# Performance work log

Hardware: AMD Instinct MI355X
Metric: run time of the kernel (lower is better)

## Reference

```python
import jax, jax.numpy as jnp
import numpy as np
from jax import lax

OC = 128      # out_channels
KS = 7        # kernel_size
STRIDE = 2
IMG = 224     # image_size
NS = 7        # num_scales
PAD = KS // 2 # 3
MAXS = 2      # max_scale
EPS = 1e-5
OUT = IMG // STRIDE  # 112
B = 32
DN = ('NCHW', 'OIHW', 'NCHW')


def _windows():
    # Mirrors the torch __init__ window construction (float32 linspace like torch).
    scales = np.linspace(2.0, 1.0, NS, dtype=np.float32)
    borders = np.linspace(0, IMG // 2, NS + 1).astype(np.int64)
    iw = np.empty((NS, 4, 4), dtype=np.int64)
    for s in range(NS):
        a, b = borders[s], borders[s + 1]
        c, d = IMG - b, IMG - a
        iw[s] = np.array([[a, a, b, c], [b, a, d, b], [c, b, d, d], [a, c, c, d]])
    ow = iw // STRIDE  # output windows
    iwp = iw + PAD * MAXS
    iwp = np.stack([(iwp[s].astype(np.float32) / scales[s]).astype(np.int64) for s in range(NS)])
    iwp[:, :, :2] -= PAD
    iwp[:, :, 2:] += PAD
    return iwp, ow

IWP, OW = _windows()


def _bn(x, g, b):
    # BatchNorm2d in training mode: biased batch stats over (N, H, W)
    m = jnp.mean(x, axis=(0, 2, 3), keepdims=True)
    v = jnp.var(x, axis=(0, 2, 3), keepdims=True)
    return g[None, :, None, None] * (x - m) * lax.rsqrt(v + EPS) + b[None, :, None, None]


def _forward(inp, conv_w, gamma1, beta1, conv2_w, gamma2, beta2):
    n = inp.shape[0]
    x = jnp.pad(inp, ((0, 0), (0, 0), (PAD, PAD), (PAD, PAD)))  # ConstantPad2d(3, 0)
    out = jnp.zeros((n, OC, OUT, OUT), inp.dtype)
    for s in range(NS):
        for w in range(4):
            ti, li, bi, ri = (int(v) for v in IWP[s, w])
            crop = x[:, :, ti:bi, li:ri]
            # torch interpolate(bilinear, antialias) to the crop's own size is the identity,
            # since input_window_sizes == (bi-ti, ri-li) exactly.
            f = lax.conv_general_dilated(crop, conv_w, (STRIDE, STRIDE), 'VALID',
                                         dimension_numbers=DN)
            to, lo, bo, ro = (int(v) for v in OW[s, w])
            oh, owid = bo - to, ro - lo
            fh, fw = f.shape[2], f.shape[3]
            # torch 'nearest' (size-based): src = floor(i * in / out)
            ih = (np.arange(oh) * fh) // oh
            iwd = (np.arange(owid) * fw) // owid
            up = f[:, :, ih][:, :, :, iwd]
            out = out.at[:, :, to:bo, lo:ro].set(up)
    h = jax.nn.relu(_bn(out, gamma1, beta1))
    # MaxPool2d(kernel=3, stride=2, padding=1) -> pads with -inf
    h = lax.reduce_window(h, jnp.asarray(-jnp.inf, h.dtype), lax.max,
                          (1, 1, 3, 3), (1, 1, 2, 2),
                          ((0, 0), (0, 0), (1, 1), (1, 1)))
    h = lax.conv_general_dilated(h, conv2_w, (1, 1), ((1, 1), (1, 1)),
                                 dimension_numbers=DN)
    return jax.nn.relu(_bn(h, gamma2, beta2))


def setup_inputs() -> dict:
    key = jax.random.key(0)
    k0, k1, k2 = jax.random.split(key, 3)
    inp = jax.random.normal(k0, (B, 3, IMG, IMG), jnp.float32)
    conv_w = jax.random.normal(k1, (OC, 3, KS, KS), jnp.float32) * 0.05
    conv2_w = jax.random.normal(k2, (OC, OC, 3, 3), jnp.float32) * 0.03
    return {
        'inp': inp,
        'conv_w': conv_w,
        'gamma1': jnp.ones((OC,), jnp.float32),
        'beta1': jnp.zeros((OC,), jnp.float32),
        'conv2_w': conv2_w,
        'gamma2': jnp.ones((OC,), jnp.float32),
        'beta2': jnp.zeros((OC,), jnp.float32),
    }


def reference(inp, conv_w, gamma1, beta1, conv2_w, gamma2, beta2):
    return _forward(inp, conv_w, gamma1, beta1, conv2_w, gamma2, beta2)
```

## Files before the change

kernel.cpp:

```cpp
#include <hip/hip_runtime.h>
#include <hip/hip_bf16.h>
#include <cstdint>

#define IMGSZ 224
#define OUTSZ 112
#define POOLSZ 56
#define OCN 128
#define BN_ 32
#define PIX1 (OUTSZ*OUTSZ)
#define PIX2 (POOLSZ*POOLSZ)
#define HP 58
#define HSTRIDE (HP*HP*OCN)
#define PW 240
#define PH 233
#define PPL (PH*PW)
#define K1C 192

typedef float f32x4 __attribute__((ext_vector_type(4)));
typedef short bf16x8 __attribute__((ext_vector_type(8)));
struct alignas(4) u4a { unsigned x, y, z, w; };

__device__ inline short f2bf(float v) {
    __hip_bfloat16 h = __float2bfloat16(v);
    return *(short*)&h;
}
__device__ inline unsigned pack2bf(float a, float b) {
    return (unsigned short)f2bf(a) | ((unsigned)(unsigned short)f2bf(b) << 16);
}
__device__ inline float bf2f(short s) {
    return __uint_as_float(((unsigned)(unsigned short)s) << 16);
}
__device__ inline bf16x8 ldb8(const short* p) {
    u4a t = *(const u4a*)p;
    union { u4a u; bf16x8 v; } c; c.u = t; return c.v;
}
__device__ inline void gload16(const short* g, short* l) {
    __builtin_amdgcn_global_load_lds((const __attribute__((address_space(1))) void*)g,
                                     (__attribute__((address_space(3))) void*)l, 16, 0, 0);
}

template<int CTRL>
__device__ inline float dppf(float v) {
    return __int_as_float(__builtin_amdgcn_update_dpp(0, __float_as_int(v), CTRL, 0xF, 0xF, true));
}
__device__ inline float rowsum16(float v) {
    v += dppf<0xB1>(v);
    v += dppf<0x4E>(v);
    v += dppf<0x141>(v);
    v += dppf<0x140>(v);
    return v;
}

__global__ __launch_bounds__(256) void k_setup(const float* __restrict__ w1,
                                               short* __restrict__ w1b,
                                               const float* __restrict__ w2,
                                               short* __restrict__ w2b,
                                               int2* __restrict__ map,
                                               float* __restrict__ stats,
                                               unsigned* __restrict__ h2p) {
    int blk = blockIdx.x;
    int tid = threadIdx.x;
    if (blk < 49) {
        int p = blk * 256 + tid;
        int oy = p / OUTSZ, ox = p % OUTSZ;
        int e = min(min(oy, ox), min(111 - oy, 111 - ox));
        int s = e >> 3;
        int a = 16 * s, b = a + 16, c = 224 - b, d = 224 - a;
        int ao = a >> 1, bo = b >> 1, co = c >> 1, dd = d >> 1;
        int ti, li, bi, ri;
        if      (oy >= ao && oy < bo && ox >= ao && ox < co) { ti=a; li=a; bi=b; ri=c; }
        else if (oy >= bo && oy < dd && ox >= ao && ox < bo) { ti=b; li=a; bi=d; ri=b; }
        else if (oy >= co && oy < dd && ox >= bo && ox < dd) { ti=c; li=b; bi=d; ri=d; }
        else                                                 { ti=a; li=c; bi=c; ri=d; }
        float scale = (float)(2.0 - (double)s * 0.16666666666666666);
        int tip = (int)((float)(ti + 6) / scale) - 3;
        int lip = (int)((float)(li + 6) / scale) - 3;
        int bip = (int)((float)(bi + 6) / scale) + 3;
        int rip = (int)((float)(ri + 6) / scale) + 3;
        int fh = (bip - tip - 7) / 2 + 1;
        int fw = (rip - lip - 7) / 2 + 1;
        int to = ti >> 1, lo = li >> 1, bo2 = bi >> 1, ro = ri >> 1;
        int i = oy - to, j = ox - lo;
        int pp = (i * fh) / (bo2 - to);
        int qq = (j * fw) / (ro - lo);
        map[p] = make_int2(tip + 2 * pp, lip + 2 * qq);
    } else if (blk < 145) {
        int idx = (blk - 49) * 256 + tid;
        int oc = idx / K1C, k = idx % K1C;
        int g8 = k >> 3, e2 = k & 7;
        float v = 0.f;
        if (g8 < 21 && e2 < 7) {
            int ic = g8 / 7, ky = g8 - ic * 7;
            v = w1[((oc * 3 + ic) * 7 + ky) * 7 + e2];
        }
        w1b[idx] = f2bf(v);
    } else if (blk < 721) {
        int idx = (blk - 145) * 256 + tid;
        int oc = idx / 1152;
        int rem = idx - oc * 1152;
        int ic = rem / 9;
        int s  = rem - ic * 9;
        int t  = s * 2 + (ic >> 6);
        int ic6 = ic & 63;
        int slot = (ic6 >> 3) ^ (oc & 7);
        w2b[t * 8192 + oc * 64 + slot * 8 + (ic6 & 7)] = f2bf(w2[idx]);
    } else if (blk < 785) {
        stats[(blk - 721) * 256 + tid] = 0.f;
    } else {
        int idx = blk - 785;
        int bx = idx % 57, n = idx / 57;
        int c2 = tid & 63, po = tid >> 6;
        int pp = bx * 4 + po;
        int y, x;
        if      (pp < 58)  { y = 0;  x = pp; }
        else if (pp < 116) { y = 57; x = pp - 58; }
        else if (pp < 172) { y = pp - 116 + 1; x = 0; }
        else               { y = pp - 172 + 1; x = 57; }
        h2p[(size_t)n * (HSTRIDE / 2) + (y * HP + x) * 64 + c2] = 0u;
    }
}

__global__ __launch_bounds__(256) void k_pad(const float* __restrict__ inp,
                                             short* __restrict__ padA,
                                             short* __restrict__ padB) {
    int x = threadIdx.x;
    if (x >= PW) return;
    int y = blockIdx.x;
    int pl = blockIdx.y;
    int iy = y - 3;
    bool yok = (unsigned)iy < 224u;
    const float* src = inp + (size_t)pl * 50176 + iy * 224;
    float vA = (yok && (unsigned)(x - 3) < 224u) ? src[x - 3] : 0.f;
    float vB = (yok && (unsigned)(x - 2) < 224u) ? src[x - 2] : 0.f;
    size_t o = (size_t)pl * PPL + y * PW + x;
    padA[o] = f2bf(vA);
    padB[o] = f2bf(vB);
}

__global__ __launch_bounds__(256, 4) void k_conv1m(const short* __restrict__ padA,
                                                   const short* __restrict__ padB,
                                                   const short* __restrict__ w1b,
                                                   const int2* __restrict__ map,
                                                   short* __restrict__ out1b,
                                                   float* __restrict__ sum1x,
                                                   float* __restrict__ sq1x) {
    __shared__ short As[64 * 256];
    __shared__ float sred[4][64][2];
    int tid = threadIdx.x;
    int wave = tid >> 6, lane = tid & 63;
    int q = lane >> 4, l16 = lane & 15;
    int id = blockIdx.x;
    int swz = (id & 7) * 784 + (id >> 3);
    int n = swz / 196;
    int x196 = swz - n * 196;
    int ochalf = x196 & 1;
    int pxblk = x196 >> 1;
    int px0 = pxblk * 128 + wave * 32 + l16;
    int px1 = px0 + 16;
    int2 m0 = map[px0];
    int2 m1 = map[px1];
    size_t bn = (size_t)n * 3 * PPL;
    const short* r0 = ((m0.y & 1) ? padB + (m0.y - 1) : padA + m0.y) + bn + m0.x * PW;
    const short* r1 = ((m1.y & 1) ? padB + (m1.y - 1) : padA + m1.y) + bn + m1.x * PW;

    const short* wsl = w1b + ochalf * 64 * K1C;
#pragma unroll
    for (int i = 0; i < 6; i++) {
        int chunk = tid + i * 256;
        int r = chunk / 24, c = chunk - r * 24;
        u4a v = *(const u4a*)(wsl + r * K1C + c * 8);
        *(u4a*)(As + r * 256 + ((c ^ (r & 15)) * 8)) = v;
    }

    bf16x8 ld[12];
#pragma unroll
    for (int icc = 0; icc < 6; icc++) {
        int g8 = (icc == 5) ? 20 : (icc * 4 + q);
        int ic = (g8 >= 7) + (g8 >= 14);
        int ky = g8 - ic * 7;
        int off = ic * PPL + ky * PW;
        ld[icc * 2]     = ldb8(r0 + off);
        ld[icc * 2 + 1] = ldb8(r1 + off);
    }

    f32x4 acc[4][2];
#pragma unroll
    for (int t = 0; t < 4; t++) { acc[t][0] = (f32x4){0,0,0,0}; acc[t][1] = (f32x4){0,0,0,0}; }

    __syncthreads();

    const short* Abase = As + l16 * 256;
#pragma unroll
    for (int icc = 0; icc < 6; icc++) {
        bf16x8 bf0 = ld[icc * 2];
        bf16x8 bf1 = ld[icc * 2 + 1];
        int pos = ((icc * 4 + q) ^ l16) * 8;
#pragma unroll
        for (int t = 0; t < 4; t++) {
            bf16x8 af = *(const bf16x8*)(Abase + t * 16 * 256 + pos);
            acc[t][0] = __builtin_amdgcn_mfma_f32_16x16x32_bf16(af, bf0, acc[t][0], 0, 0, 0);
            acc[t][1] = __builtin_amdgcn_mfma_f32_16x16x32_bf16(af, bf1, acc[t][1], 0, 0, 0);
        }
    }

    short* ob = out1b + ((size_t)(n * PIX1) + px0) * OCN + ochalf * 64 + q * 4;
#pragma unroll
    for (int t = 0; t < 4; t++) {
#pragma unroll
        for (int g = 0; g < 2; g++) {
            f32x4 a = acc[t][g];
            uint2 u;
            u.x = pack2bf(a[0], a[1]);
            u.y = pack2bf(a[2], a[3]);
            *(uint2*)(ob + (size_t)g * 16 * OCN + t * 16) = u;
        }
    }

#pragma unroll
    for (int t = 0; t < 4; t++) {
#pragma unroll
        for (int r = 0; r < 4; r++) {
            float a0 = acc[t][0][r], a1 = acc[t][1][r];
            float s = rowsum16(a0 + a1);
            float z = rowsum16(fmaf(a0, a0, a1 * a1));
            if (l16 == 0) {
                int ocl = t * 16 + q * 4 + r;
                sred[wave][ocl][0] = s;
                sred[wave][ocl][1] = z;
            }
        }
    }
    __syncthreads();
    if (tid < 64) {
        float s = sred[0][tid][0] + sred[1][tid][0] + sred[2][tid][0] + sred[3][tid][0];
        float z = sred[0][tid][1] + sred[1][tid][1] + sred[2][tid][1] + sred[3][tid][1];
        int oc = ochalf * 64 + tid;
        atomicAdd(&sum1x[n * OCN + oc], s);
        atomicAdd(&sq1x[n * OCN + oc], z);
    }
}

__global__ void k_fin2(const float* __restrict__ sumx, const float* __restrict__ sqx,
                       const float* __restrict__ gamma, const float* __restrict__ beta,
                       float invN, float* __restrict__ scale, float* __restrict__ shift) {
    int c = threadIdx.x;
    if (c >= OCN) return;
    float s = 0.f, q = 0.f;
    for (int n = 0; n < BN_; n++) { s += sumx[n * OCN + c]; q += sqx[n * OCN + c]; }
    float m = s * invN;
    float v = q * invN - m * m;
    float sc = gamma[c] * rsqrtf(v + 1e-5f);
    scale[c] = sc;
    shift[c] = beta[c] - m * sc;
}

__global__ __launch_bounds__(256) void k_bnpool(const unsigned* __restrict__ out1b,
                                                const float* __restrict__ scale,
                                                const float* __restrict__ shift,
                                                unsigned* __restrict__ h2p) {
    int tid = threadIdx.x;
    int c2 = tid & 63, po = tid >> 6;
    int pp = blockIdx.x * 4 + po;
    int n = blockIdx.y;
    int py = pp / POOLSZ, px = pp % POOLSZ;
    const unsigned* base = out1b + (size_t)n * PIX1 * 64;
    float sc0 = scale[2 * c2],     sh0 = shift[2 * c2];
    float sc1 = scale[2 * c2 + 1], sh1 = shift[2 * c2 + 1];
    float m0 = -1e30f, m1 = -1e30f;
#pragma unroll
    for (int dy = 0; dy < 3; dy++) {
        int y = 2 * py - 1 + dy;
        if ((unsigned)y >= (unsigned)OUTSZ) continue;
#pragma unroll
        for (int dx = 0; dx < 3; dx++) {
            int x = 2 * px - 1 + dx;
            if ((unsigned)x >= (unsigned)OUTSZ) continue;
            unsigned u = base[(size_t)(y * OUTSZ + x) * 64 + c2];
            float v0 = __uint_as_float(u << 16);
            float v1 = __uint_as_float(u & 0xffff0000u);
            m0 = fmaxf(m0, fmaf(sc0, v0, sh0));
            m1 = fmaxf(m1, fmaf(sc1, v1, sh1));
        }
    }
    m0 = fmaxf(m0, 0.f); m1 = fmaxf(m1, 0.f);
    h2p[(size_t)n * (HSTRIDE / 2) + ((py + 1) * HP + (px + 1)) * 64 + c2] = pack2bf(m0, m1);
}

__global__ __launch_bounds__(256, 4) void k_conv2g(const short* __restrict__ h2p,
                                                   const short* __restrict__ w2b,
                                                   short* __restrict__ out2b,
                                                   float* __restrict__ sum2x,
                                                   float* __restrict__ sq2x) {
    __shared__ short LDSb[15360];
    int tid = threadIdx.x;
    int wave = tid >> 6, lane = tid & 63;
    int q = lane >> 4, l16 = lane & 15;
    int id = blockIdx.x;
    int xcd = id & 7, seq = id >> 3;
    int n = xcd + 8 * (seq / 28);
    int rb = seq % 28;
    int y0 = rb * 2;
    const short* hb = h2p + (size_t)n * HSTRIDE;

    int bofs[4];
#pragma unroll
    for (int i = 0; i < 4; i++) {
        int ck = tid + i * 256;
        if (ck > 895) ck = 895;
        int px = ck >> 3, sl = ck & 7;
        int r = px >= 56;
        int xc = px - (r ? 56 : 0);
        bofs[i] = ((y0 + r) * 58 + xc) * 128 + ((sl ^ (px & 7)) * 8);
    }

    f32x4 acc[2][7];
#pragma unroll
    for (int t16 = 0; t16 < 2; t16++)
#pragma unroll
        for (int g = 0; g < 7; g++) acc[t16][g] = (f32x4){0, 0, 0, 0};

    const short* Az = LDSb;
    const short* Bz = LDSb + 8192;
    int arow0 = (wave * 32 + l16) * 64;
    int arow1 = arow0 + 16 * 64;

    for (int t = 0; t < 18; t++) {
        __syncthreads();
        const short* wt = w2b + t * 8192;
#pragma unroll
        for (int i = 0; i < 4; i++)
            gload16(wt + (tid + i * 256) * 8, &LDSb[(tid + i * 256) * 8]);
        int s = t >> 1, ich = t & 1;
        int dy = s / 3, dx = s - dy * 3;
        int doff = (dy * 58 + dx) * 128 + ich * 64;
#pragma unroll
        for (int i = 0; i < 3; i++)
            gload16(hb + bofs[i] + doff, &LDSb[8192 + (tid + i * 256) * 8]);
        if (tid < 128)
            gload16(hb + bofs[3] + doff, &LDSb[8192 + (tid + 768) * 8]);
        asm volatile("s_waitcnt vmcnt(0)" ::: "memory");
        __syncthreads();
#pragma unroll
        for (int icc2 = 0; icc2 < 2; icc2++) {
            int so = ((icc2 * 4 + q) ^ (l16 & 7)) * 8;
            bf16x8 af0 = *(const bf16x8*)(Az + arow0 + so);
            bf16x8 af1 = *(const bf16x8*)(Az + arow1 + so);
            bf16x8 bf[7];
#pragma unroll
            for (int g = 0; g < 7; g++)
                bf[g] = *(const bf16x8*)(Bz + (g * 16 + l16) * 64 + so);
#pragma unroll
            for (int g = 0; g < 7; g++) {
                acc[0][g] = __builtin_amdgcn_mfma_f32_16x16x32_bf16(af0, bf[g], acc[0][g], 0, 0, 0);
                acc[1][g] = __builtin_amdgcn_mfma_f32_16x16x32_bf16(af1, bf[g], acc[1][g], 0, 0, 0);
            }
        }
    }

    short* ob = out2b + ((size_t)n * PIX2 + y0 * 56) * OCN + wave * 32 + q * 4;
#pragma unroll
    for (int t16 = 0; t16 < 2; t16++) {
#pragma unroll
        for (int g = 0; g < 7; g++) {
            f32x4 a = acc[t16][g];
            uint2 u;
            u.x = pack2bf(a[0], a[1]);
            u.y = pack2bf(a[2], a[3]);
            *(uint2*)(ob + (size_t)(g * 16 + l16) * OCN + t16 * 16) = u;
        }
    }

#pragma unroll
    for (int t16 = 0; t16 < 2; t16++) {
#pragma unroll
        for (int r = 0; r < 4; r++) {
            float sv = 0.f, zv = 0.f;
#pragma unroll
            for (int g = 0; g < 7; g++) {
                float v = acc[t16][g][r];
                sv += v;
                zv = fmaf(v, v, zv);
            }
            sv = rowsum16(sv);
            zv = rowsum16(zv);
            if (l16 == 0) {
                int oc = wave * 32 + t16 * 16 + q * 4 + r;
                atomicAdd(&sum2x[n * OCN + oc], sv);
                atomicAdd(&sq2x[n * OCN + oc], zv);
            }
        }
    }
}

__global__ __launch_bounds__(256) void k_bnrelu(const short* __restrict__ in2,
                                                float* __restrict__ y,
                                                const float* __restrict__ scale,
                                                const float* __restrict__ shift) {
    int tid = threadIdx.x;
    int w = tid >> 6, l = tid & 63;
    int pxg = blockIdx.x * 256 + w * 64 + (l & 15) * 4;
    int n = pxg / PIX2;
    int px = pxg - n * PIX2;
    const short* src = in2 + (size_t)pxg * OCN + (l >> 4) * 8;
    float* dst = y + (size_t)n * (OCN * PIX2) + px;
#pragma unroll
    for (int jc = 0; jc < 4; jc++) {
        int c0 = (l >> 4) * 8 + jc * 32;
        bf16x8 v0 = ldb8(src + jc * 32);
        bf16x8 v1 = ldb8(src + OCN + jc * 32);
        bf16x8 v2 = ldb8(src + 2 * OCN + jc * 32);
        bf16x8 v3 = ldb8(src + 3 * OCN + jc * 32);
#pragma unroll
        for (int j = 0; j < 8; j++) {
            float sc = scale[c0 + j], sh = shift[c0 + j];
            float4 o;
            o.x = fmaxf(fmaf(sc, bf2f(v0[j]), sh), 0.f);
            o.y = fmaxf(fmaf(sc, bf2f(v1[j]), sh), 0.f);
            o.z = fmaxf(fmaf(sc, bf2f(v2[j]), sh), 0.f);
            o.w = fmaxf(fmaf(sc, bf2f(v3[j]), sh), 0.f);
            *(float4*)(dst + (size_t)(c0 + j) * PIX2) = o;
        }
    }
}

extern "C" void kernel_launch(void* const* d_in, const int* in_sizes, int n_in,
                              void* d_out, int out_size, void* d_ws, size_t ws_size,
                              hipStream_t stream) {
    const float* inp = (const float*)d_in[0];
    const float* w1  = (const float*)d_in[1];
    const float* g1  = (const float*)d_in[2];
    const float* b1  = (const float*)d_in[3];
    const float* w2  = (const float*)d_in[4];
    const float* g2  = (const float*)d_in[5];
    const float* b2  = (const float*)d_in[6];
    float* out = (float*)d_out;

    char* ws = (char*)d_ws;
    int2*  map   = (int2*)ws;
    float* stats = (float*)(ws + 102400);
    short* w2b   = (short*)(ws + 176128);
    short* w1b   = (short*)(ws + 471040);
    short* padA  = (short*)(ws + 520192);
    short* padB  = (short*)(ws + 11256832ULL);
    short* h2p   = (short*)(ws + 21993472ULL);
    short* out1b = (short*)(ws + 49551360ULL);
    short* out2b = (short*)(ws + 152311808ULL);

    float* sum1x = stats;
    float* sq1x  = stats + 4096;
    float* sum2x = stats + 8192;
    float* sq2x  = stats + 12288;
    float* SC1 = stats + 16384, *SH1 = stats + 16512;
    float* SC2 = stats + 16640, *SH2 = stats + 16768;

    k_setup <<<dim3(2609), 256, 0, stream>>>(w1, w1b, w2, w2b, map, stats, (unsigned*)h2p);
    k_pad   <<<dim3(PH, 96), 256, 0, stream>>>(inp, padA, padB);
    k_conv1m<<<dim3(6272), 256, 0, stream>>>(padA, padB, w1b, map, out1b, sum1x, sq1x);
    k_fin2  <<<1, 128, 0, stream>>>(sum1x, sq1x, g1, b1, 1.f / (BN_ * PIX1), SC1, SH1);
    k_bnpool<<<dim3(PIX2 / 4, BN_), 256, 0, stream>>>((const unsigned*)out1b, SC1, SH1, (unsigned*)h2p);
    k_conv2g<<<dim3(896), 256, 0, stream>>>(h2p, w2b, out2b, sum2x, sq2x);
    k_fin2  <<<1, 128, 0, stream>>>(sum2x, sq2x, g2, b2, 1.f / (BN_ * PIX2), SC2, SH2);
    k_bnrelu<<<dim3(392), 256, 0, stream>>>(out2b, out, SC2, SH2);
}
```

Before: 250.5 us.

## Fuse pad into setup, load conv1 weights from global, widen bnpool

```diff
diff --git a/kernel.cpp b/kernel.cpp
--- a/kernel.cpp
+++ b/kernel.cpp
@@ -57,9 +57,27 @@
                                                short* __restrict__ w2b,
                                                int2* __restrict__ map,
                                                float* __restrict__ stats,
-                                               unsigned* __restrict__ h2p) {
+                                               unsigned* __restrict__ h2p,
+                                               const float* __restrict__ inp,
+                                               short* __restrict__ padA,
+                                               short* __restrict__ padB) {
     int blk = blockIdx.x;
     int tid = threadIdx.x;
+    if (blk >= 2609) {
+        int idx = blk - 2609;
+        int pl = idx / PH, y = idx - (idx / PH) * PH;
+        int x = tid;
+        if (x >= PW) return;
+        int iy = y - 3;
+        bool yok = (unsigned)iy < 224u;
+        const float* src = inp + (size_t)pl * 50176 + iy * 224;
+        float vA = (yok && (unsigned)(x - 3) < 224u) ? src[x - 3] : 0.f;
+        float vB = (yok && (unsigned)(x - 2) < 224u) ? src[x - 2] : 0.f;
+        size_t o = (size_t)pl * PPL + y * PW + x;
+        padA[o] = f2bf(vA);
+        padB[o] = f2bf(vB);
+        return;
+    }
     if (blk < 49) {
         int p = blk * 256 + tid;
         int oy = p / OUTSZ, ox = p % OUTSZ;
@@ -120,23 +138,6 @@
     }
 }
 
-__global__ __launch_bounds__(256) void k_pad(const float* __restrict__ inp,
-                                             short* __restrict__ padA,
-                                             short* __restrict__ padB) {
-    int x = threadIdx.x;
-    if (x >= PW) return;
-    int y = blockIdx.x;
-    int pl = blockIdx.y;
-    int iy = y - 3;
-    bool yok = (unsigned)iy < 224u;
-    const float* src = inp + (size_t)pl * 50176 + iy * 224;
-    float vA = (yok && (unsigned)(x - 3) < 224u) ? src[x - 3] : 0.f;
-    float vB = (yok && (unsigned)(x - 2) < 224u) ? src[x - 2] : 0.f;
-    size_t o = (size_t)pl * PPL + y * PW + x;
-    padA[o] = f2bf(vA);
-    padB[o] = f2bf(vB);
-}
-
 __global__ __launch_bounds__(256, 4) void k_conv1m(const short* __restrict__ padA,
                                                    const short* __restrict__ padB,
                                                    const short* __restrict__ w1b,
@@ -144,7 +145,6 @@
                                                    short* __restrict__ out1b,
                                                    float* __restrict__ sum1x,
                                                    float* __restrict__ sq1x) {
-    __shared__ short As[64 * 256];
     __shared__ float sred[4][64][2];
     int tid = threadIdx.x;
     int wave = tid >> 6, lane = tid & 63;
@@ -163,15 +163,6 @@
     const short* r0 = ((m0.y & 1) ? padB + (m0.y - 1) : padA + m0.y) + bn + m0.x * PW;
     const short* r1 = ((m1.y & 1) ? padB + (m1.y - 1) : padA + m1.y) + bn + m1.x * PW;
 
-    const short* wsl = w1b + ochalf * 64 * K1C;
-#pragma unroll
-    for (int i = 0; i < 6; i++) {
-        int chunk = tid + i * 256;
-        int r = chunk / 24, c = chunk - r * 24;
-        u4a v = *(const u4a*)(wsl + r * K1C + c * 8);
-        *(u4a*)(As + r * 256 + ((c ^ (r & 15)) * 8)) = v;
-    }
-
     bf16x8 ld[12];
 #pragma unroll
     for (int icc = 0; icc < 6; icc++) {
@@ -183,21 +174,19 @@
         ld[icc * 2 + 1] = ldb8(r1 + off);
     }
 
+    const short* wsl = w1b + ochalf * 64 * K1C + l16 * K1C + q * 8;
+
     f32x4 acc[4][2];
 #pragma unroll
     for (int t = 0; t < 4; t++) { acc[t][0] = (f32x4){0,0,0,0}; acc[t][1] = (f32x4){0,0,0,0}; }
 
-    __syncthreads();
-
-    const short* Abase = As + l16 * 256;
 #pragma unroll
     for (int icc = 0; icc < 6; icc++) {
         bf16x8 bf0 = ld[icc * 2];
         bf16x8 bf1 = ld[icc * 2 + 1];
-        int pos = ((icc * 4 + q) ^ l16) * 8;
 #pragma unroll
         for (int t = 0; t < 4; t++) {
-            bf16x8 af = *(const bf16x8*)(Abase + t * 16 * 256 + pos);
+            bf16x8 af = ldb8(wsl + t * 16 * K1C + icc * 32);
             acc[t][0] = __builtin_amdgcn_mfma_f32_16x16x32_bf16(af, bf0, acc[t][0], 0, 0, 0);
             acc[t][1] = __builtin_amdgcn_mfma_f32_16x16x32_bf16(af, bf1, acc[t][1], 0, 0, 0);
         }
@@ -254,19 +243,20 @@
     shift[c] = beta[c] - m * sc;
 }
 
-__global__ __launch_bounds__(256) void k_bnpool(const unsigned* __restrict__ out1b,
+__global__ __launch_bounds__(256) void k_bnpool(const uint2* __restrict__ out1b,
                                                 const float* __restrict__ scale,
                                                 const float* __restrict__ shift,
-                                                unsigned* __restrict__ h2p) {
+                                                uint2* __restrict__ h2p) {
     int tid = threadIdx.x;
-    int c2 = tid & 63, po = tid >> 6;
-    int pp = blockIdx.x * 4 + po;
+    int c4 = tid & 31, po = tid >> 5;
+    int pp = blockIdx.x * 8 + po;
     int n = blockIdx.y;
     int py = pp / POOLSZ, px = pp % POOLSZ;
-    const unsigned* base = out1b + (size_t)n * PIX1 * 64;
-    float sc0 = scale[2 * c2],     sh0 = shift[2 * c2];
-    float sc1 = scale[2 * c2 + 1], sh1 = shift[2 * c2 + 1];
-    float m0 = -1e30f, m1 = -1e30f;
+    const uint2* base = out1b + (size_t)n * PIX1 * 32;
+    int c0 = c4 * 4;
+    float4 sc = *(const float4*)(scale + c0);
+    float4 sh = *(const float4*)(shift + c0);
+    float m0 = -1e30f, m1 = -1e30f, m2 = -1e30f, m3 = -1e30f;
 #pragma unroll
     for (int dy = 0; dy < 3; dy++) {
         int y = 2 * py - 1 + dy;
@@ -275,15 +265,17 @@
         for (int dx = 0; dx < 3; dx++) {
             int x = 2 * px - 1 + dx;
             if ((unsigned)x >= (unsigned)OUTSZ) continue;
-            unsigned u = base[(size_t)(y * OUTSZ + x) * 64 + c2];
-            float v0 = __uint_as_float(u << 16);
-            float v1 = __uint_as_float(u & 0xffff0000u);
-            m0 = fmaxf(m0, fmaf(sc0, v0, sh0));
-            m1 = fmaxf(m1, fmaf(sc1, v1, sh1));
-        }
-    }
-    m0 = fmaxf(m0, 0.f); m1 = fmaxf(m1, 0.f);
-    h2p[(size_t)n * (HSTRIDE / 2) + ((py + 1) * HP + (px + 1)) * 64 + c2] = pack2bf(m0, m1);
+            uint2 u = base[(size_t)(y * OUTSZ + x) * 32 + c4];
+            m0 = fmaxf(m0, fmaf(sc.x, __uint_as_float(u.x << 16), sh.x));
+            m1 = fmaxf(m1, fmaf(sc.y, __uint_as_float(u.x & 0xffff0000u), sh.y));
+            m2 = fmaxf(m2, fmaf(sc.z, __uint_as_float(u.y << 16), sh.z));
+            m3 = fmaxf(m3, fmaf(sc.w, __uint_as_float(u.y & 0xffff0000u), sh.w));
+        }
+    }
+    uint2 o;
+    o.x = pack2bf(fmaxf(m0, 0.f), fmaxf(m1, 0.f));
+    o.y = pack2bf(fmaxf(m2, 0.f), fmaxf(m3, 0.f));
+    h2p[(size_t)n * (HSTRIDE / 4) + ((py + 1) * HP + (px + 1)) * 32 + c4] = o;
 }
 
 __global__ __launch_bounds__(256, 4) void k_conv2g(const short* __restrict__ h2p,
@@ -453,11 +445,11 @@
     float* SC1 = stats + 16384, *SH1 = stats + 16512;
     float* SC2 = stats + 16640, *SH2 = stats + 16768;
 
-    k_setup <<<dim3(2609), 256, 0, stream>>>(w1, w1b, w2, w2b, map, stats, (unsigned*)h2p);
-    k_pad   <<<dim3(PH, 96), 256, 0, stream>>>(inp, padA, padB);
+    k_setup <<<dim3(2609 + PH * 96), 256, 0, stream>>>(w1, w1b, w2, w2b, map, stats,
+                                                       (unsigned*)h2p, inp, padA, padB);
     k_conv1m<<<dim3(6272), 256, 0, stream>>>(padA, padB, w1b, map, out1b, sum1x, sq1x);
     k_fin2  <<<1, 128, 0, stream>>>(sum1x, sq1x, g1, b1, 1.f / (BN_ * PIX1), SC1, SH1);
-    k_bnpool<<<dim3(PIX2 / 4, BN_), 256, 0, stream>>>((const unsigned*)out1b, SC1, SH1, (unsigned*)h2p);
+    k_bnpool<<<dim3(PIX2 / 8, BN_), 256, 0, stream>>>((const uint2*)out1b, SC1, SH1, (uint2*)h2p);
     k_conv2g<<<dim3(896), 256, 0, stream>>>(h2p, w2b, out2b, sum2x, sq2x);
     k_fin2  <<<1, 128, 0, stream>>>(sum2x, sq2x, g2, b2, 1.f / (BN_ * PIX2), SC2, SH2);
     k_bnrelu<<<dim3(392), 256, 0, stream>>>(out2b, out, SC2, SH2);
```

Measured after the change: 284.8 us. +13.7%, slower.
